# Kernel optimization log

Measured on AMD Instinct MI355X. Metric: run time of the kernel, lower is better.

Reference implementation:

```python
import jax, jax.numpy as jnp
import numpy as np

KEEP_P = 0.75  # 1 - dropout_p, dropout_p = 0.25

def setup_inputs() -> dict:
    key = jax.random.key(0)
    k1, k2, k3, k4 = jax.random.split(key, 4)
    B, Sq, Skv, D, Dv = 8, 2048, 2048, 128, 128
    x1 = jax.random.normal(k1, (B, Sq, D), dtype=jnp.float32)
    x2 = jax.random.normal(k2, (B, Skv, D), dtype=jnp.float32)
    x3 = jax.random.normal(k3, (B, Skv, Dv), dtype=jnp.float32)
    # torch Dropout(p): mask = bernoulli(keep_p) / keep_p
    keep = jax.random.bernoulli(k4, KEEP_P, (B, Sq, Skv))
    dropout_mask = keep.astype(jnp.float32) / KEEP_P
    return {"x1": x1, "x2": x2, "x3": x3, "dropout_mask": dropout_mask}

def reference(x1, x2, x3, dropout_mask):
    # scores: [B, Sq, Skv] = x1 @ x2^T (no scale: scale_factor is None)
    scores = jnp.einsum("bqd,bkd->bqk", x1, x2)
    probs = jax.nn.softmax(scores, axis=-1)
    probs = probs * dropout_mask  # dropout with fixed mask
    out = jnp.einsum("bqk,bkv->bqv", probs, x3)  # [B, Sq, Dv]
    return out
```

## Files before the change

kernel.cpp:

```cpp
#include <hip/hip_runtime.h>
#include <stdint.h>

#define SQ 2048
#define SKV 2048
#define DD 128
#define NB 8
#define LOG2E 1.44269504088896340736f
#define M0L 57.70780163555852f

typedef float    f4v __attribute__((ext_vector_type(4)));
typedef __bf16   bf8 __attribute__((ext_vector_type(8)));
typedef _Float16 h8  __attribute__((ext_vector_type(8)));

__device__ __forceinline__ void async16(const void* g, void* l) {
    __builtin_amdgcn_global_load_lds(
        (const __attribute__((address_space(1))) void*)g,
        (__attribute__((address_space(3))) void*)l, 16, 0, 0);
}

__global__ void preprocess(const float* __restrict__ x2, _Float16* __restrict__ Kh,
                           const float* __restrict__ x3, __bf16* __restrict__ VTf) {
    __shared__ __bf16 tile[32][33];
    const int bid = blockIdx.x;
    if (bid < 1024) {
        int tid = bid * 256 + threadIdx.x;
        int d8 = tid & 15;
        int kv = (tid >> 4) & (SKV - 1);
        int b  = tid >> 15;
        const float* p = x2 + ((size_t)b * SKV + kv) * DD + d8 * 8;
        f4v a0 = *(const f4v*)p;
        f4v a1 = *(const f4v*)(p + 4);
        h8 h;
#pragma unroll
        for (int c = 0; c < 4; c++) {
            h[c]     = (_Float16)a0[c];
            h[c + 4] = (_Float16)a1[c];
        }
        int s = d8 >> 2, g = d8 & 3, kb32 = kv >> 5, row = kv & 31;
        *(h8*)(Kh + (size_t)(b * 64 + kb32) * 4096 + (size_t)((s * 32 + row) * 4 + g) * 8) = h;
    } else {
        int t = bid - 1024;
        int kb32 = t & 63, dv0 = ((t >> 6) & 3) * 32, b = t >> 8;
        int tx = threadIdx.x & 31, ty = threadIdx.x >> 5;
        const float* src = x3 + ((size_t)b * SKV + kb32 * 32 + ty) * DD + dv0 + tx;
#pragma unroll
        for (int i = 0; i < 32; i += 8)
            tile[ty + i][tx] = (__bf16)src[(size_t)i * DD];
        __syncthreads();
        int pcol = (tx < 16) ? ((tx >> 2) << 3) + (tx & 3)
                             : (((tx - 16) >> 2) << 3) + 4 + (tx & 3);
        __bf16* dst = VTf + (size_t)(b * 64 + kb32) * 4096 + pcol;
#pragma unroll
        for (int i = 0; i < 32; i += 8)
            dst[(size_t)(dv0 + ty + i) * 32] = tile[tx][ty + i];
    }
}

__global__ __launch_bounds__(256, 2) void attn_kernel(
    const float* __restrict__ Qf, const _Float16* __restrict__ Kh,
    const __bf16* __restrict__ Vt, const float* __restrict__ mask,
    float* __restrict__ O_part, float* __restrict__ l_part,
    int nsp, int kv_len) {
    __shared__ __align__(16) char smem[3][16384];
    const int lin = blockIdx.x;
    const int per_xcd = (NB * nsp) >> 3;
    const int xcd = lin & 7;
    const int idx = lin >> 3;
    const int slice = xcd * per_xcd + (idx >> 4);
    const int qblk = idx & 15;
    const int b = slice / nsp, sid = slice % nsp;
    const int tid = threadIdx.x;
    const int w = tid >> 6, lane = tid & 63;
    const int g = lane >> 4, n = lane & 15;
    const int qb = qblk * 128 + w * 32;
    const int kv0 = sid * kv_len;
    const int kb32_0 = kv0 >> 5;
    const int niter = kv_len >> 5;

    const _Float16* Kt0 = Kh + (size_t)(b * 64 + kb32_0) * 4096;
    const __bf16*   Vt0 = Vt + (size_t)(b * 64 + kb32_0) * 4096;
    auto stageTo = [&](char* buf, int it) {
#pragma unroll
        for (int jj = 0; jj < 4; jj++) {
            int j = w * 4 + jj;
            if (j < 8)
                async16(Kt0 + (size_t)it * 4096 + j * 512 + lane * 8,
                        (void*)(buf + j * 1024));
            else
                async16(Vt0 + (size_t)it * 4096 + (j - 8) * 512 + lane * 8,
                        (void*)(buf + 8192 + (j - 8) * 1024));
        }
    };

    h8 qf[2][4];
#pragma unroll
    for (int u = 0; u < 2; u++) {
        const float* Qrow = Qf + ((size_t)b * SQ + qb + u * 16 + n) * DD + g * 8;
#pragma unroll
        for (int s = 0; s < 4; s++) {
            f4v v0 = *(const f4v*)(Qrow + s * 32);
            f4v v1 = *(const f4v*)(Qrow + s * 32 + 4);
#pragma unroll
            for (int c = 0; c < 4; c++) {
                qf[u][s][c]     = (_Float16)v0[c];
                qf[u][s][c + 4] = (_Float16)v1[c];
            }
        }
    }

    const float* mrow0 = mask + ((size_t)b * SQ + qb + n) * SKV + kv0;
    const float* mrow1 = mrow0 + (size_t)16 * SKV;

    const f4v zero = {0.f, 0.f, 0.f, 0.f};
    f4v o0[8], o1[8];
#pragma unroll
    for (int t = 0; t < 8; t++) { o0[t] = zero; o1[t] = zero; }
    float l0 = 0.f, l1 = 0.f;

    char* s0p = &smem[0][0];
    char* s1p = &smem[1][0];
    char* s2p = &smem[2][0];

    stageTo(s0p, 0);
    asm volatile("" ::: "memory");
    f4v mA00 = *(const f4v*)(mrow0 + g * 4);
    f4v mA01 = *(const f4v*)(mrow0 + 16 + g * 4);
    f4v mA10 = *(const f4v*)(mrow1 + g * 4);
    f4v mA11 = *(const f4v*)(mrow1 + 16 + g * 4);
    asm volatile("" ::: "memory");
    const int it1 = (1 < niter) ? 1 : 0;
    stageTo(s1p, it1);
    asm volatile("" ::: "memory");
    f4v mB00 = *(const f4v*)(mrow0 + it1 * 32 + g * 4);
    f4v mB01 = *(const f4v*)(mrow0 + it1 * 32 + 16 + g * 4);
    f4v mB10 = *(const f4v*)(mrow1 + it1 * 32 + g * 4);
    f4v mB11 = *(const f4v*)(mrow1 + it1 * 32 + 16 + g * 4);
    f4v mC00 = zero, mC01 = zero, mC10 = zero, mC11 = zero;

    auto body = [&](int it, const char* bufR, char* bufW,
                    const f4v& u00, const f4v& u01, const f4v& u10, const f4v& u11,
                    f4v& t00, f4v& t01, f4v& t10, f4v& t11) {
        asm volatile("s_waitcnt vmcnt(8)" ::: "memory");
        __builtin_amdgcn_s_barrier();
        asm volatile("" ::: "memory");
        const int itp = (it + 2 < niter) ? it + 2 : niter - 1;
        stageTo(bufW, itp);
        t00 = *(const f4v*)(mrow0 + itp * 32 + g * 4);
        t01 = *(const f4v*)(mrow0 + itp * 32 + 16 + g * 4);
        t10 = *(const f4v*)(mrow1 + itp * 32 + g * 4);
        t11 = *(const f4v*)(mrow1 + itp * 32 + 16 + g * 4);

        const _Float16* Lk = (const _Float16*)bufR;
        const __bf16*   Lv = (const __bf16*)(bufR + 8192);

        f4v s00 = zero, s01 = zero, s10 = zero, s11 = zero;
#pragma unroll
        for (int s = 0; s < 4; s++) {
            h8 a0 = *(const h8*)(Lk + (size_t)((s * 32 + n) * 4 + g) * 8);
            h8 a1 = *(const h8*)(Lk + (size_t)((s * 32 + n + 16) * 4 + g) * 8);
            s00 = __builtin_amdgcn_mfma_f32_16x16x32_f16(a0, qf[0][s], s00, 0, 0, 0);
            s01 = __builtin_amdgcn_mfma_f32_16x16x32_f16(a1, qf[0][s], s01, 0, 0, 0);
            s10 = __builtin_amdgcn_mfma_f32_16x16x32_f16(a0, qf[1][s], s10, 0, 0, 0);
            s11 = __builtin_amdgcn_mfma_f32_16x16x32_f16(a1, qf[1][s], s11, 0, 0, 0);
        }

        bf8 pf0, pf1;
#pragma unroll
        for (int r = 0; r < 4; r++) {
            float e00 = exp2f(s00[r] * LOG2E - M0L);
            float e01 = exp2f(s01[r] * LOG2E - M0L);
            float e10 = exp2f(s10[r] * LOG2E - M0L);
            float e11 = exp2f(s11[r] * LOG2E - M0L);
            l0 += e00 + e01;
            l1 += e10 + e11;
            pf0[r]     = (__bf16)(e00 * u00[r]);
            pf0[r + 4] = (__bf16)(e01 * u01[r]);
            pf1[r]     = (__bf16)(e10 * u10[r]);
            pf1[r + 4] = (__bf16)(e11 * u11[r]);
        }

#pragma unroll
        for (int t = 0; t < 8; t++) {
            bf8 vf = *(const bf8*)(Lv + (size_t)((t * 16 + n) * 4 + g) * 8);
            o0[t] = __builtin_amdgcn_mfma_f32_16x16x32_bf16(pf0, vf, o0[t], 0, 0, 0);
            o1[t] = __builtin_amdgcn_mfma_f32_16x16x32_bf16(pf1, vf, o1[t], 0, 0, 0);
        }
    };

    for (int it = 0; it < niter; it += 3) {
        body(it,     s0p, s2p, mA00, mA01, mA10, mA11, mC00, mC01, mC10, mC11);
        if (it + 1 < niter)
            body(it + 1, s1p, s0p, mB00, mB01, mB10, mB11, mA00, mA01, mA10, mA11);
        if (it + 2 < niter)
            body(it + 2, s2p, s1p, mC00, mC01, mC10, mC11, mB00, mB01, mB10, mB11);
    }

    l0 += __shfl_xor(l0, 16); l0 += __shfl_xor(l0, 32);
    l1 += __shfl_xor(l1, 16); l1 += __shfl_xor(l1, 32);
    const int qt = qblk * 8 + w * 2;
    const int tile0 = (b * 128 + qt) * nsp + sid;
    const int tile1 = (b * 128 + qt + 1) * nsp + sid;
    float* op0 = O_part + (size_t)tile0 * 2048;
    float* op1 = O_part + (size_t)tile1 * 2048;
#pragma unroll
    for (int t = 0; t < 8; t++)
#pragma unroll
        for (int r = 0; r < 4; r++) {
            op0[(g * 4 + r) * 128 + t * 16 + n] = o0[t][r];
            op1[(g * 4 + r) * 128 + t * 16 + n] = o1[t][r];
        }
    if (g == 0) {
        l_part[(size_t)tile0 * 16 + n] = l0;
        l_part[(size_t)tile1 * 16 + n] = l1;
    }
}

__global__ __launch_bounds__(256) void combine_kernel(
    const float* __restrict__ O_part, const float* __restrict__ l_part,
    float* __restrict__ out, int nsp) {
    const int qt = blockIdx.x;
    const int b  = blockIdx.y;
    const int tbase = (b * 128 + qt) * nsp;
    const int q  = threadIdx.x >> 4;
    const int d8 = threadIdx.x & 15;
    f4v a0 = {0.f, 0.f, 0.f, 0.f}, a1 = {0.f, 0.f, 0.f, 0.f};
    float L = 0.f;
    for (int s = 0; s < nsp; s++) {
        const float* op = O_part + (size_t)(tbase + s) * 2048 + q * 128 + d8 * 8;
        a0 += *(const f4v*)op;
        a1 += *(const f4v*)(op + 4);
        L  += l_part[(size_t)(tbase + s) * 16 + q];
    }
    float scale = 1.0f / L;
    float* o = out + ((size_t)b * SQ + qt * 16 + q) * DD + d8 * 8;
    *(f4v*)o       = a0 * scale;
    *(f4v*)(o + 4) = a1 * scale;
}

extern "C" void kernel_launch(void* const* d_in, const int* in_sizes, int n_in,
                              void* d_out, int out_size, void* d_ws, size_t ws_size,
                              hipStream_t stream) {
    const float* x1   = (const float*)d_in[0];
    const float* x2   = (const float*)d_in[1];
    const float* x3   = (const float*)d_in[2];
    const float* mask = (const float*)d_in[3];
    float* out = (float*)d_out;

    const size_t kelems = (size_t)NB * SKV * DD;
    _Float16* Kh  = (_Float16*)d_ws;
    __bf16*   VTf = (__bf16*)(Kh + kelems);
    float*    O_part = (float*)(VTf + kelems);

    size_t base = 2 * kelems * 2;
    size_t per  = (size_t)NB * 128 * (2048 + 16) * sizeof(float);
    int nsp = 4;
    while (nsp > 1 && base + (size_t)nsp * per > ws_size) nsp >>= 1;
    float* l_part = O_part + (size_t)NB * 128 * nsp * 2048;

    hipLaunchKernelGGL(preprocess, dim3(3072), dim3(256), 0, stream,
                       x2, Kh, x3, VTf);
    hipLaunchKernelGGL(attn_kernel, dim3(16 * NB * nsp), dim3(256), 0, stream,
                       x1, Kh, VTf, mask, O_part, l_part, nsp, SKV / nsp);
    hipLaunchKernelGGL(combine_kernel, dim3(128, NB), dim3(256), 0, stream,
                       O_part, l_part, out, nsp);
}
```

Before: 233.8 us.

## Fuse split-KV combine into attention kernel via last-block atomic counter

Drops the separate combine kernel. Each attention block now increments a per-(batch, query-block) atomic counter after writing its partial output. The last block to arrive sums the partial O and l values across the KV splits and writes the normalized output. This saves a kernel launch and its gap, and the final reduction can overlap with attention blocks still running, at the cost of a memset launch, thread fences, and a serialized tail inside the final blocks.

```diff
diff --git a/kernel.cpp b/kernel.cpp
--- a/kernel.cpp
+++ b/kernel.cpp
@@ -60,8 +60,10 @@
     const float* __restrict__ Qf, const _Float16* __restrict__ Kh,
     const __bf16* __restrict__ Vt, const float* __restrict__ mask,
     float* __restrict__ O_part, float* __restrict__ l_part,
+    unsigned* __restrict__ counters, float* __restrict__ out,
     int nsp, int kv_len) {
     __shared__ __align__(16) char smem[3][16384];
+    __shared__ unsigned oldv_s;
     const int lin = blockIdx.x;
     const int per_xcd = (NB * nsp) >> 3;
     const int xcd = lin & 7;
@@ -213,28 +215,33 @@
         l_part[(size_t)tile0 * 16 + n] = l0;
         l_part[(size_t)tile1 * 16 + n] = l1;
     }
-}
-
-__global__ __launch_bounds__(256) void combine_kernel(
-    const float* __restrict__ O_part, const float* __restrict__ l_part,
-    float* __restrict__ out, int nsp) {
-    const int qt = blockIdx.x;
-    const int b  = blockIdx.y;
-    const int tbase = (b * 128 + qt) * nsp;
-    const int q  = threadIdx.x >> 4;
-    const int d8 = threadIdx.x & 15;
-    f4v a0 = {0.f, 0.f, 0.f, 0.f}, a1 = {0.f, 0.f, 0.f, 0.f};
-    float L = 0.f;
-    for (int s = 0; s < nsp; s++) {
-        const float* op = O_part + (size_t)(tbase + s) * 2048 + q * 128 + d8 * 8;
-        a0 += *(const f4v*)op;
-        a1 += *(const f4v*)(op + 4);
-        L  += l_part[(size_t)(tbase + s) * 16 + q];
-    }
-    float scale = 1.0f / L;
-    float* o = out + ((size_t)b * SQ + qt * 16 + q) * DD + d8 * 8;
-    *(f4v*)o       = a0 * scale;
-    *(f4v*)(o + 4) = a1 * scale;
+
+    __threadfence();
+    __syncthreads();
+    if (tid == 0) oldv_s = atomicAdd(&counters[b * 16 + qblk], 1u);
+    __syncthreads();
+    if (oldv_s == (unsigned)(nsp - 1)) {
+        __threadfence();
+        const int row = tid >> 1;
+        const int c0  = (tid & 1) * 64;
+        const int qtt = qblk * 8 + (row >> 4);
+        const int r16 = row & 15;
+        f4v acc[16];
+#pragma unroll
+        for (int v = 0; v < 16; v++) acc[v] = zero;
+        float L = 0.f;
+        for (int s = 0; s < nsp; s++) {
+            const size_t tile = (size_t)((b * 128 + qtt) * nsp + s);
+            const float* op = O_part + tile * 2048 + r16 * 128 + c0;
+#pragma unroll
+            for (int v = 0; v < 16; v++) acc[v] += *(const f4v*)(op + v * 4);
+            L += l_part[tile * 16 + r16];
+        }
+        float scale = 1.0f / L;
+        float* o = out + ((size_t)b * SQ + qblk * 128 + row) * DD + c0;
+#pragma unroll
+        for (int v = 0; v < 16; v++) *(f4v*)(o + v * 4) = acc[v] * scale;
+    }
 }
 
 extern "C" void kernel_launch(void* const* d_in, const int* in_sizes, int n_in,
@@ -254,13 +261,14 @@
     size_t base = 2 * kelems * 2;
     size_t per  = (size_t)NB * 128 * (2048 + 16) * sizeof(float);
     int nsp = 4;
-    while (nsp > 1 && base + (size_t)nsp * per > ws_size) nsp >>= 1;
-    float* l_part = O_part + (size_t)NB * 128 * nsp * 2048;
-
+    while (nsp > 1 && base + (size_t)nsp * per + 4096 > ws_size) nsp >>= 1;
+    float*    l_part   = O_part + (size_t)NB * 128 * nsp * 2048;
+    unsigned* counters = (unsigned*)(l_part + (size_t)NB * 128 * nsp * 16);
+
+    hipMemsetAsync(counters, 0, NB * 16 * sizeof(unsigned), stream);
     hipLaunchKernelGGL(preprocess, dim3(3072), dim3(256), 0, stream,
                        x2, Kh, x3, VTf);
     hipLaunchKernelGGL(attn_kernel, dim3(16 * NB * nsp), dim3(256), 0, stream,
-                       x1, Kh, VTf, mask, O_part, l_part, nsp, SKV / nsp);
-    hipLaunchKernelGGL(combine_kernel, dim3(128, NB), dim3(256), 0, stream,
-                       O_part, l_part, out, nsp);
-}
+                       x1, Kh, VTf, mask, O_part, l_part, counters, out,
+                       nsp, SKV / nsp);
+}
```

New measurement: 330.7 us. +41.4%, slower.

## Drop split-KV partials and combine kernel; one block per 64 query rows

Applied to the files above, without the earlier changes.

The attention kernel now covers the full KV range per block, with 16 query rows per wave. It normalizes in-kernel and writes the output directly, so the O_part/l_part workspace and the combine launch are gone. The preprocess kernel also rearranges the K and V tile layouts so the LDS fragment reads index contiguously by lane. The aim is to remove partial-output traffic and a kernel launch. In exchange, the grid becomes 256 blocks with launch bounds of one block per CU, K/V reuse per wave is halved, and there are fewer resident waves to hide mask-load latency.

```diff
diff --git a/kernel.cpp b/kernel.cpp
--- a/kernel.cpp
+++ b/kernel.cpp
@@ -37,7 +37,8 @@
             h[c + 4] = (_Float16)a1[c];
         }
         int s = d8 >> 2, g = d8 & 3, kb32 = kv >> 5, row = kv & 31;
-        *(h8*)(Kh + (size_t)(b * 64 + kb32) * 4096 + (size_t)((s * 32 + row) * 4 + g) * 8) = h;
+        int h8idx = s * 128 + ((row >> 4) << 6) + g * 16 + (row & 15);
+        *(h8*)(Kh + (size_t)(b * 64 + kb32) * 4096 + (size_t)h8idx * 8) = h;
     } else {
         int t = bid - 1024;
         int kb32 = t & 63, dv0 = ((t >> 6) & 3) * 32, b = t >> 8;
@@ -49,36 +50,32 @@
         __syncthreads();
         int pcol = (tx < 16) ? ((tx >> 2) << 3) + (tx & 3)
                              : (((tx - 16) >> 2) << 3) + 4 + (tx & 3);
-        __bf16* dst = VTf + (size_t)(b * 64 + kb32) * 4096 + pcol;
-#pragma unroll
-        for (int i = 0; i < 32; i += 8)
-            dst[(size_t)(dv0 + ty + i) * 32] = tile[tx][ty + i];
+        __bf16* base = VTf + (size_t)(b * 64 + kb32) * 4096
+                     + ((pcol >> 3) << 7) + (pcol & 7);
+#pragma unroll
+        for (int i = 0; i < 32; i += 8) {
+            int dv = dv0 + ty + i;
+            base[((dv >> 4) << 9) + ((dv & 15) << 3)] = tile[tx][ty + i];
+        }
     }
 }
 
-__global__ __launch_bounds__(256, 2) void attn_kernel(
+__global__ __launch_bounds__(256, 1) void attn_kernel(
     const float* __restrict__ Qf, const _Float16* __restrict__ Kh,
     const __bf16* __restrict__ Vt, const float* __restrict__ mask,
-    float* __restrict__ O_part, float* __restrict__ l_part,
-    int nsp, int kv_len) {
+    float* __restrict__ out) {
     __shared__ __align__(16) char smem[3][16384];
     const int lin = blockIdx.x;
-    const int per_xcd = (NB * nsp) >> 3;
-    const int xcd = lin & 7;
-    const int idx = lin >> 3;
-    const int slice = xcd * per_xcd + (idx >> 4);
-    const int qblk = idx & 15;
-    const int b = slice / nsp, sid = slice % nsp;
+    const int b = lin & 7;
+    const int qblk = lin >> 3;
     const int tid = threadIdx.x;
     const int w = tid >> 6, lane = tid & 63;
     const int g = lane >> 4, n = lane & 15;
-    const int qb = qblk * 128 + w * 32;
-    const int kv0 = sid * kv_len;
-    const int kb32_0 = kv0 >> 5;
-    const int niter = kv_len >> 5;
-
-    const _Float16* Kt0 = Kh + (size_t)(b * 64 + kb32_0) * 4096;
-    const __bf16*   Vt0 = Vt + (size_t)(b * 64 + kb32_0) * 4096;
+    const int qb = qblk * 64 + w * 16;
+    const int niter = SKV / 32;
+
+    const _Float16* Kt0 = Kh + (size_t)b * 64 * 4096;
+    const __bf16*   Vt0 = Vt + (size_t)b * 64 * 4096;
     auto stageTo = [&](char* buf, int it) {
 #pragma unroll
         for (int jj = 0; jj < 4; jj++) {
@@ -92,30 +89,26 @@
         }
     };
 
-    h8 qf[2][4];
-#pragma unroll
-    for (int u = 0; u < 2; u++) {
-        const float* Qrow = Qf + ((size_t)b * SQ + qb + u * 16 + n) * DD + g * 8;
-#pragma unroll
-        for (int s = 0; s < 4; s++) {
-            f4v v0 = *(const f4v*)(Qrow + s * 32);
-            f4v v1 = *(const f4v*)(Qrow + s * 32 + 4);
-#pragma unroll
-            for (int c = 0; c < 4; c++) {
-                qf[u][s][c]     = (_Float16)v0[c];
-                qf[u][s][c + 4] = (_Float16)v1[c];
-            }
+    const float* Qrow = Qf + ((size_t)b * SQ + qb + n) * DD + g * 8;
+    h8 qf[4];
+#pragma unroll
+    for (int s = 0; s < 4; s++) {
+        f4v v0 = *(const f4v*)(Qrow + s * 32);
+        f4v v1 = *(const f4v*)(Qrow + s * 32 + 4);
+#pragma unroll
+        for (int c = 0; c < 4; c++) {
+            qf[s][c]     = (_Float16)v0[c];
+            qf[s][c + 4] = (_Float16)v1[c];
         }
     }
 
-    const float* mrow0 = mask + ((size_t)b * SQ + qb + n) * SKV + kv0;
-    const float* mrow1 = mrow0 + (size_t)16 * SKV;
+    const float* mrow = mask + ((size_t)b * SQ + qb + n) * SKV;
 
     const f4v zero = {0.f, 0.f, 0.f, 0.f};
-    f4v o0[8], o1[8];
-#pragma unroll
-    for (int t = 0; t < 8; t++) { o0[t] = zero; o1[t] = zero; }
-    float l0 = 0.f, l1 = 0.f;
+    f4v o_acc[8];
+#pragma unroll
+    for (int t = 0; t < 8; t++) o_acc[t] = zero;
+    float l_run = 0.f;
 
     char* s0p = &smem[0][0];
     char* s1p = &smem[1][0];
@@ -123,118 +116,74 @@
 
     stageTo(s0p, 0);
     asm volatile("" ::: "memory");
-    f4v mA00 = *(const f4v*)(mrow0 + g * 4);
-    f4v mA01 = *(const f4v*)(mrow0 + 16 + g * 4);
-    f4v mA10 = *(const f4v*)(mrow1 + g * 4);
-    f4v mA11 = *(const f4v*)(mrow1 + 16 + g * 4);
+    f4v mA0 = *(const f4v*)(mrow + g * 4);
+    f4v mA1 = *(const f4v*)(mrow + 16 + g * 4);
     asm volatile("" ::: "memory");
-    const int it1 = (1 < niter) ? 1 : 0;
-    stageTo(s1p, it1);
+    stageTo(s1p, 1);
     asm volatile("" ::: "memory");
-    f4v mB00 = *(const f4v*)(mrow0 + it1 * 32 + g * 4);
-    f4v mB01 = *(const f4v*)(mrow0 + it1 * 32 + 16 + g * 4);
-    f4v mB10 = *(const f4v*)(mrow1 + it1 * 32 + g * 4);
-    f4v mB11 = *(const f4v*)(mrow1 + it1 * 32 + 16 + g * 4);
-    f4v mC00 = zero, mC01 = zero, mC10 = zero, mC11 = zero;
+    f4v mB0 = *(const f4v*)(mrow + 32 + g * 4);
+    f4v mB1 = *(const f4v*)(mrow + 48 + g * 4);
+    f4v mC0 = zero, mC1 = zero;
 
     auto body = [&](int it, const char* bufR, char* bufW,
-                    const f4v& u00, const f4v& u01, const f4v& u10, const f4v& u11,
-                    f4v& t00, f4v& t01, f4v& t10, f4v& t11) {
-        asm volatile("s_waitcnt vmcnt(8)" ::: "memory");
+                    const f4v& u0, const f4v& u1, f4v& t0, f4v& t1) {
+        asm volatile("s_waitcnt vmcnt(6)" ::: "memory");
         __builtin_amdgcn_s_barrier();
         asm volatile("" ::: "memory");
         const int itp = (it + 2 < niter) ? it + 2 : niter - 1;
         stageTo(bufW, itp);
-        t00 = *(const f4v*)(mrow0 + itp * 32 + g * 4);
-        t01 = *(const f4v*)(mrow0 + itp * 32 + 16 + g * 4);
-        t10 = *(const f4v*)(mrow1 + itp * 32 + g * 4);
-        t11 = *(const f4v*)(mrow1 + itp * 32 + 16 + g * 4);
+        t0 = *(const f4v*)(mrow + itp * 32 + g * 4);
+        t1 = *(const f4v*)(mrow + itp * 32 + 16 + g * 4);
 
         const _Float16* Lk = (const _Float16*)bufR;
         const __bf16*   Lv = (const __bf16*)(bufR + 8192);
 
-        f4v s00 = zero, s01 = zero, s10 = zero, s11 = zero;
+        f4v sa0 = zero, sa1 = zero;
 #pragma unroll
         for (int s = 0; s < 4; s++) {
-            h8 a0 = *(const h8*)(Lk + (size_t)((s * 32 + n) * 4 + g) * 8);
-            h8 a1 = *(const h8*)(Lk + (size_t)((s * 32 + n + 16) * 4 + g) * 8);
-            s00 = __builtin_amdgcn_mfma_f32_16x16x32_f16(a0, qf[0][s], s00, 0, 0, 0);
-            s01 = __builtin_amdgcn_mfma_f32_16x16x32_f16(a1, qf[0][s], s01, 0, 0, 0);
-            s10 = __builtin_amdgcn_mfma_f32_16x16x32_f16(a0, qf[1][s], s10, 0, 0, 0);
-            s11 = __builtin_amdgcn_mfma_f32_16x16x32_f16(a1, qf[1][s], s11, 0, 0, 0);
-        }
-
-        bf8 pf0, pf1;
+            h8 a0 = *(const h8*)(Lk + (size_t)(s * 128 + g * 16 + n) * 8);
+            h8 a1 = *(const h8*)(Lk + (size_t)(s * 128 + 64 + g * 16 + n) * 8);
+            sa0 = __builtin_amdgcn_mfma_f32_16x16x32_f16(a0, qf[s], sa0, 0, 0, 0);
+            sa1 = __builtin_amdgcn_mfma_f32_16x16x32_f16(a1, qf[s], sa1, 0, 0, 0);
+        }
+
+        bf8 pf;
 #pragma unroll
         for (int r = 0; r < 4; r++) {
-            float e00 = exp2f(s00[r] * LOG2E - M0L);
-            float e01 = exp2f(s01[r] * LOG2E - M0L);
-            float e10 = exp2f(s10[r] * LOG2E - M0L);
-            float e11 = exp2f(s11[r] * LOG2E - M0L);
-            l0 += e00 + e01;
-            l1 += e10 + e11;
-            pf0[r]     = (__bf16)(e00 * u00[r]);
-            pf0[r + 4] = (__bf16)(e01 * u01[r]);
-            pf1[r]     = (__bf16)(e10 * u10[r]);
-            pf1[r + 4] = (__bf16)(e11 * u11[r]);
+            float e0 = exp2f(sa0[r] * LOG2E - M0L);
+            float e1 = exp2f(sa1[r] * LOG2E - M0L);
+            l_run += e0 + e1;
+            pf[r]     = (__bf16)(e0 * u0[r]);
+            pf[r + 4] = (__bf16)(e1 * u1[r]);
         }
 
 #pragma unroll
         for (int t = 0; t < 8; t++) {
-            bf8 vf = *(const bf8*)(Lv + (size_t)((t * 16 + n) * 4 + g) * 8);
-            o0[t] = __builtin_amdgcn_mfma_f32_16x16x32_bf16(pf0, vf, o0[t], 0, 0, 0);
-            o1[t] = __builtin_amdgcn_mfma_f32_16x16x32_bf16(pf1, vf, o1[t], 0, 0, 0);
+            bf8 vf = *(const bf8*)(Lv + (size_t)(t * 64 + g * 16 + n) * 8);
+            o_acc[t] = __builtin_amdgcn_mfma_f32_16x16x32_bf16(pf, vf, o_acc[t], 0, 0, 0);
         }
     };
 
     for (int it = 0; it < niter; it += 3) {
-        body(it,     s0p, s2p, mA00, mA01, mA10, mA11, mC00, mC01, mC10, mC11);
+        body(it,     s0p, s2p, mA0, mA1, mC0, mC1);
         if (it + 1 < niter)
-            body(it + 1, s1p, s0p, mB00, mB01, mB10, mB11, mA00, mA01, mA10, mA11);
+            body(it + 1, s1p, s0p, mB0, mB1, mA0, mA1);
         if (it + 2 < niter)
-            body(it + 2, s2p, s1p, mC00, mC01, mC10, mC11, mB00, mB01, mB10, mB11);
+            body(it + 2, s2p, s1p, mC0, mC1, mB0, mB1);
     }
 
-    l0 += __shfl_xor(l0, 16); l0 += __shfl_xor(l0, 32);
-    l1 += __shfl_xor(l1, 16); l1 += __shfl_xor(l1, 32);
-    const int qt = qblk * 8 + w * 2;
-    const int tile0 = (b * 128 + qt) * nsp + sid;
-    const int tile1 = (b * 128 + qt + 1) * nsp + sid;
-    float* op0 = O_part + (size_t)tile0 * 2048;
-    float* op1 = O_part + (size_t)tile1 * 2048;
+    l_run += __shfl_xor(l_run, 16);
+    l_run += __shfl_xor(l_run, 32);
+    float sc[4];
+#pragma unroll
+    for (int r = 0; r < 4; r++)
+        sc[r] = 1.0f / __shfl(l_run, g * 4 + r);
+    float* orow = out + ((size_t)b * SQ + qb + g * 4) * DD + n;
 #pragma unroll
     for (int t = 0; t < 8; t++)
 #pragma unroll
-        for (int r = 0; r < 4; r++) {
-            op0[(g * 4 + r) * 128 + t * 16 + n] = o0[t][r];
-            op1[(g * 4 + r) * 128 + t * 16 + n] = o1[t][r];
-        }
-    if (g == 0) {
-        l_part[(size_t)tile0 * 16 + n] = l0;
-        l_part[(size_t)tile1 * 16 + n] = l1;
-    }
-}
-
-__global__ __launch_bounds__(256) void combine_kernel(
-    const float* __restrict__ O_part, const float* __restrict__ l_part,
-    float* __restrict__ out, int nsp) {
-    const int qt = blockIdx.x;
-    const int b  = blockIdx.y;
-    const int tbase = (b * 128 + qt) * nsp;
-    const int q  = threadIdx.x >> 4;
-    const int d8 = threadIdx.x & 15;
-    f4v a0 = {0.f, 0.f, 0.f, 0.f}, a1 = {0.f, 0.f, 0.f, 0.f};
-    float L = 0.f;
-    for (int s = 0; s < nsp; s++) {
-        const float* op = O_part + (size_t)(tbase + s) * 2048 + q * 128 + d8 * 8;
-        a0 += *(const f4v*)op;
-        a1 += *(const f4v*)(op + 4);
-        L  += l_part[(size_t)(tbase + s) * 16 + q];
-    }
-    float scale = 1.0f / L;
-    float* o = out + ((size_t)b * SQ + qt * 16 + q) * DD + d8 * 8;
-    *(f4v*)o       = a0 * scale;
-    *(f4v*)(o + 4) = a1 * scale;
+        for (int r = 0; r < 4; r++)
+            orow[(size_t)r * DD + t * 16] = o_acc[t][r] * sc[r];
 }
 
 extern "C" void kernel_launch(void* const* d_in, const int* in_sizes, int n_in,
@@ -249,18 +198,9 @@
     const size_t kelems = (size_t)NB * SKV * DD;
     _Float16* Kh  = (_Float16*)d_ws;
     __bf16*   VTf = (__bf16*)(Kh + kelems);
-    float*    O_part = (float*)(VTf + kelems);
-
-    size_t base = 2 * kelems * 2;
-    size_t per  = (size_t)NB * 128 * (2048 + 16) * sizeof(float);
-    int nsp = 4;
-    while (nsp > 1 && base + (size_t)nsp * per > ws_size) nsp >>= 1;
-    float* l_part = O_part + (size_t)NB * 128 * nsp * 2048;
 
     hipLaunchKernelGGL(preprocess, dim3(3072), dim3(256), 0, stream,
                        x2, Kh, x3, VTf);
-    hipLaunchKernelGGL(attn_kernel, dim3(16 * NB * nsp), dim3(256), 0, stream,
-                       x1, Kh, VTf, mask, O_part, l_part, nsp, SKV / nsp);
-    hipLaunchKernelGGL(combine_kernel, dim3(128, NB), dim3(256), 0, stream,
-                       O_part, l_part, out, nsp);
-}
+    hipLaunchKernelGGL(attn_kernel, dim3(256), dim3(256), 0, stream,
+                       x1, Kh, VTf, mask, out);
+}
```

After: 253.4 us. 1.08x slower.
